# Performance work log

Hardware: AMD Instinct MI355X
Metric: run time of the kernel (lower is better)

## Reference

```python
import jax, jax.numpy as jnp
import numpy as np
import math

B, S, D, H, G = 2, 2048, 2048, 16, 4
DH = D // H          # 128 head dim
BASE = 1_000_000.0   # RoPE base


def _rope(x):
    # x: (..., S, DH); interleaved RoPE matching the torch module
    pos = jnp.arange(S, dtype=jnp.float32)[:, None]            # (S,1)
    i = jnp.arange(DH // 2, dtype=jnp.float32)                 # (DH/2,)
    omega = jnp.exp(-2.0 * i / DH * math.log(BASE))            # (DH/2,)
    ang = pos * omega                                          # (S, DH/2)
    sin = jnp.repeat(jnp.sin(ang), 2, axis=-1)                 # (S, DH)
    cos = jnp.repeat(jnp.cos(ang), 2, axis=-1)                 # (S, DH)
    xe, xo = x[..., 0::2], x[..., 1::2]
    rot = jnp.stack([-xo, xe], axis=-1).reshape(x.shape)       # (-x1,x0,-x3,x2,...)
    return x * cos + rot * sin


def setup_inputs() -> dict:
    key = jax.random.key(0)
    ks = jax.random.split(key, 5)
    x = jax.random.normal(ks[0], (B, S, D), jnp.float32)
    wq = jax.random.normal(ks[1], (D, D), jnp.float32) * 0.02
    wk = jax.random.normal(ks[2], (DH * G, D), jnp.float32) * 0.02
    wv = jax.random.normal(ks[3], (DH * G, D), jnp.float32) * 0.02
    wo = jax.random.normal(ks[4], (D, D), jnp.float32) * 0.02
    bq = jnp.zeros((D,), jnp.float32)
    bk = jnp.zeros((DH * G,), jnp.float32)
    bv = jnp.zeros((DH * G,), jnp.float32)
    bo = jnp.zeros((D,), jnp.float32)
    masked = jnp.broadcast_to(jnp.triu(jnp.ones((S, S), bool), 1), (B * H, S, S))
    return {"x": x, "wq": wq, "bq": bq, "wk": wk, "bk": bk, "wv": wv,
            "bv": bv, "wo": wo, "bo": bo, "masked": masked}


def reference(x, wq, bq, wk, bk, wv, bv, wo, bo, masked):
    r = H // G  # q heads per kv head; repeat_interleave order -> q head h uses kv h//r
    q = (x @ wq.T + bq).reshape(B, S, H, DH).transpose(0, 2, 1, 3)   # (B,H,S,DH)
    k = (x @ wk.T + bk).reshape(B, S, G, DH).transpose(0, 2, 1, 3)   # (B,G,S,DH)
    v = (x @ wv.T + bv).reshape(B, S, G, DH).transpose(0, 2, 1, 3)   # (B,G,S,DH)
    q = _rope(q)
    k = _rope(k)
    qg = q.reshape(B, G, r, S, DH)                                    # group q heads by kv head
    scores = jnp.einsum('bgrsd,bgtd->bgrst', qg, k)                   # (B,G,r,S,S)
    m = masked.reshape(B, G, r, S, S)
    scores = jnp.where(m, -jnp.inf, scores)
    attn = jax.nn.softmax(scores / math.sqrt(DH), axis=-1)
    out = jnp.einsum('bgrst,bgtd->bgrsd', attn, v)                    # (B,G,r,S,DH)
    out = out.reshape(B, H, S, DH).transpose(0, 2, 1, 3).reshape(B, S, D)
    return out @ wo.T + bo
```

## Files before the change

kernel.cpp:

```cpp
#include <hip/hip_runtime.h>

typedef unsigned short u16;
typedef __attribute__((ext_vector_type(4))) float f32x4;
typedef __attribute__((ext_vector_type(8))) __bf16 bf16x8;

static __device__ __forceinline__ u16 f2bf(float f) {
  unsigned u = __float_as_uint(f);
  u += 0x7FFFu + ((u >> 16) & 1u);
  return (u16)(u >> 16);
}
static __device__ __forceinline__ float bf2f(u16 h) {
  return __uint_as_float(((unsigned)h) << 16);
}

#define GLOAD16(gsrc, ldst)                                                    \
  __builtin_amdgcn_global_load_lds(                                            \
      (const __attribute__((address_space(1))) unsigned int*)(gsrc),           \
      (__attribute__((address_space(3))) unsigned int*)(ldst), 16, 0, 0)

__global__ void k_cvt5(const float* __restrict__ x, const float* __restrict__ wq,
                       const float* __restrict__ wk, const float* __restrict__ wv,
                       const float* __restrict__ wo, const float* __restrict__ bq,
                       const float* __restrict__ bk, const float* __restrict__ bv,
                       u16* __restrict__ xb, u16* __restrict__ wqkvb,
                       u16* __restrict__ wob, float* __restrict__ biascat) {
  int i = blockIdx.x * blockDim.x + threadIdx.x;
  const float* src;
  u16* dst;
  if (i < 2097152) { src = x + (size_t)i * 4; dst = xb + (size_t)i * 4; }
  else if (i < 3145728) { src = wq + (size_t)(i - 2097152) * 4; dst = wqkvb + (size_t)(i - 2097152) * 4; }
  else if (i < 3407872) { src = wk + (size_t)(i - 3145728) * 4; dst = wqkvb + (size_t)(i - 2097152) * 4; }
  else if (i < 3670016) { src = wv + (size_t)(i - 3407872) * 4; dst = wqkvb + (size_t)(i - 2097152) * 4; }
  else if (i < 4718592) { src = wo + (size_t)(i - 3670016) * 4; dst = wob + (size_t)(i - 3670016) * 4; }
  else {
    int t = i - 4718592;
    const float* s2 = (t < 512) ? bq + t * 4
                     : (t < 640) ? bk + (t - 512) * 4
                                 : bv + (t - 640) * 4;
    ((float4*)biascat)[t] = *(const float4*)s2;
    return;
  }
  float4 v = *(const float4*)src;
  ushort4 o;
  o.x = f2bf(v.x); o.y = f2bf(v.y); o.z = f2bf(v.z); o.w = f2bf(v.w);
  *(ushort4*)dst = o;
}

template <int MODE>
__global__ __launch_bounds__(256) void k_gemm_bt(const u16* __restrict__ A,
                                                 const u16* __restrict__ Bt,
                                                 const float* __restrict__ bias,
                                                 void* __restrict__ Cv,
                                                 u16* __restrict__ VtG,
                                                 int M, int N, int K) {
  __shared__ __align__(128) char smem[16384];
  const int tid = threadIdx.x;
  const int lane = tid & 63;
  const int wave = tid >> 6;
  const int m0 = blockIdx.y << 7;
  const int n0 = blockIdx.x << 7;
  const int wr = (wave >> 1) << 6;
  const int wc = (wave & 1) << 6;

  f32x4 acc[4][4];
#pragma unroll
  for (int m = 0; m < 4; ++m)
#pragma unroll
    for (int n = 0; n < 4; ++n) acc[m][n] = (f32x4){0.f, 0.f, 0.f, 0.f};

  const int nk = K >> 5;
  for (int kt = 0; kt < nk; ++kt) {
    const int kk0 = kt << 5;
#pragma unroll
    for (int iss = 0; iss < 4; ++iss) {
      int o = tid * 16 + iss * 4096;
      int lo = o & 8191;
      int row = lo >> 6;
      int cs = ((lo >> 4) & 3) ^ (row & 3);
      const u16* src =
          (o >= 8192 ? Bt + (size_t)(n0 + row) * K : A + (size_t)(m0 + row) * K) + kk0 + cs * 8;
      GLOAD16(src, smem + iss * 4096 + wave * 1024);
    }
    __syncthreads();
    bf16x8 af[4], bfr[4];
#pragma unroll
    for (int m = 0; m < 4; ++m) {
      int r = wr + m * 16 + (lane & 15);
      af[m] = *(const bf16x8*)(smem + r * 64 + (((lane >> 4) ^ (r & 3)) << 4));
    }
#pragma unroll
    for (int n = 0; n < 4; ++n) {
      int r = wc + n * 16 + (lane & 15);
      bfr[n] = *(const bf16x8*)(smem + 8192 + r * 64 + (((lane >> 4) ^ (r & 3)) << 4));
    }
#pragma unroll
    for (int m = 0; m < 4; ++m)
#pragma unroll
      for (int n = 0; n < 4; ++n)
        acc[m][n] = __builtin_amdgcn_mfma_f32_16x16x32_bf16(af[m], bfr[n], acc[m][n], 0, 0, 0);
    __syncthreads();
  }

  if (MODE == 2 && n0 >= 2560) {
#pragma unroll
    for (int n = 0; n < 4; ++n) {
      int col = n0 + wc + n * 16 + (lane & 15);
      int vd = col - 2560;
      float bsv = bias[col];
      u16* vrow = VtG + ((size_t)vd) * 2048;
#pragma unroll
      for (int m = 0; m < 4; ++m) {
        int rb = m0 + wr + m * 16 + ((lane >> 4) << 2);
        int bb = rb >> 11, ss = rb & 2047;
        ushort4 w;
        w.x = f2bf(acc[m][n][0] + bsv);
        w.y = f2bf(acc[m][n][1] + bsv);
        w.z = f2bf(acc[m][n][2] + bsv);
        w.w = f2bf(acc[m][n][3] + bsv);
        *(ushort4*)(vrow + (size_t)bb * (512 * 2048) + ss) = w;
      }
    }
    return;
  }

  if (MODE == 2) {
#pragma unroll
    for (int n = 0; n < 4; ++n) {
      int col = n0 + wc + n * 16 + (lane & 15);
      float bsv = bias[col];
      float omega = __expf(-0.21586735f * (float)((col & 127) >> 1));
      float sd1, cd1, sd2, cd2, sd3, cd3;
      sincosf(omega, &sd1, &cd1);
      sincosf(omega * 2.f, &sd2, &cd2);
      sincosf(omega * 3.f, &sd3, &cd3);
      const bool odd = col & 1;
      const float qsc = (col < 2048) ? 0.08838834764831845f : 1.0f;
#pragma unroll
      for (int m = 0; m < 4; ++m) {
        int rb = m0 + wr + m * 16 + ((lane >> 4) << 2);
        float s0, c0;
        sincosf((float)(rb & 2047) * omega, &s0, &c0);
        float css[4] = {c0, c0 * cd1 - s0 * sd1, c0 * cd2 - s0 * sd2, c0 * cd3 - s0 * sd3};
        float snn[4] = {s0, s0 * cd1 + c0 * sd1, s0 * cd2 + c0 * sd2, s0 * cd3 + c0 * sd3};
#pragma unroll
        for (int j = 0; j < 4; ++j) {
          float v = acc[m][n][j] + bsv;
          float partner = __shfl_xor(v, 1);
          float r = odd ? fmaf(v, css[j], partner * snn[j])
                        : fmaf(v, css[j], -partner * snn[j]);
          ((u16*)Cv)[(size_t)(rb + j) * N + col] = f2bf(r * qsc);
        }
      }
    }
    return;
  }

#pragma unroll
  for (int n = 0; n < 4; ++n) {
    int col = n0 + wc + n * 16 + (lane & 15);
    float bsv = bias[col];
#pragma unroll
    for (int m = 0; m < 4; ++m) {
      int rb = m0 + wr + m * 16 + ((lane >> 4) << 2);
#pragma unroll
      for (int j = 0; j < 4; ++j) {
        float v = acc[m][n][j] + bsv;
        ((float*)Cv)[(size_t)(rb + j) * N + col] = v;
      }
    }
  }
}

__global__ __launch_bounds__(256) void k_attn(const u16* __restrict__ qkv,
                                              const u16* __restrict__ vtg,
                                              u16* __restrict__ Ob) {
  __shared__ __align__(128) char smem[40960];
  const int tid = threadIdx.x, lane = tid & 63, wave = tid >> 6;
  const int g16 = lane >> 4;
  const int l15 = lane & 15;
  const int bh = blockIdx.x;
  const int Q0 = (31 - blockIdx.y) << 6;
  const int b = bh >> 4, h = bh & 15, gq = h >> 2;
  const int brow = b << 11;
  const int qcol = h << 7;
  const int kcol = 2048 + (gq << 7);
  const u16* vt_base = vtg + ((size_t)((b << 2) + gq) << 7) * 2048;

  bf16x8 qf[4];
  {
    int qrow = brow + Q0 + wave * 16 + l15;
    const u16* qp = qkv + (size_t)qrow * 3072 + qcol + (g16 << 3);
#pragma unroll
    for (int kk = 0; kk < 4; ++kk) qf[kk] = *(const bf16x8*)(qp + kk * 32);
  }

  f32x4 oacc[8];
#pragma unroll
  for (int d = 0; d < 8; ++d) oacc[d] = (f32x4){0.f, 0.f, 0.f, 0.f};
  float mrow[4], lrow[4];
#pragma unroll
  for (int j = 0; j < 4; ++j) { mrow[j] = -1e30f; lrow[j] = 0.f; }

  const int nkt = (Q0 >> 6) + 1;
  char* const pbase = smem + 32768 + wave * 2048;

  for (int kt = 0; kt < nkt; ++kt) {
    const size_t krowg = (size_t)(brow + (kt << 6));
#pragma unroll
    for (int iss = 0; iss < 4; ++iss) {
      int o = iss * 4096 + tid * 16;
      int row = o >> 8;
      int cs = ((o >> 4) & 15) ^ (row & 7);
      const u16* src = qkv + (krowg + row) * 3072 + kcol + cs * 8;
      GLOAD16(src, smem + iss * 4096 + wave * 1024);
    }
#pragma unroll
    for (int iss = 0; iss < 4; ++iss) {
      int o = iss * 4096 + tid * 16;
      int d = o >> 7;
      int cs = ((o >> 4) & 7) ^ (d & 7);
      const u16* src = vt_base + (size_t)d * 2048 + (kt << 6) + cs * 8;
      GLOAD16(src, smem + 16384 + iss * 4096 + wave * 1024);
    }
    __syncthreads();

    f32x4 sfr[4];
    __builtin_amdgcn_s_setprio(1);
#pragma unroll
    for (int kc = 0; kc < 4; ++kc) {
      f32x4 s = (f32x4){0.f, 0.f, 0.f, 0.f};
      int r = kc * 16 + l15;
#pragma unroll
      for (int kk = 0; kk < 4; ++kk) {
        int byte = r * 256 + ((((kk << 2) + g16) ^ (r & 7)) << 4);
        bf16x8 kf = *(const bf16x8*)(smem + byte);
        s = __builtin_amdgcn_mfma_f32_16x16x32_bf16(qf[kk], kf, s, 0, 0, 0);
      }
      sfr[kc] = s;
    }
    __builtin_amdgcn_s_setprio(0);
    const int qbase = Q0 + wave * 16 + (g16 << 2);
#pragma unroll
    for (int kc = 0; kc < 4; ++kc) {
      int kidx = (kt << 6) + kc * 16 + l15;
#pragma unroll
      for (int j = 0; j < 4; ++j)
        if (kidx > qbase + j) sfr[kc][j] = -3.0e38f;
    }
#pragma unroll
    for (int j = 0; j < 4; ++j) {
      float mx = fmaxf(fmaxf(sfr[0][j], sfr[1][j]), fmaxf(sfr[2][j], sfr[3][j]));
#pragma unroll
      for (int msk = 8; msk >= 1; msk >>= 1) mx = fmaxf(mx, __shfl_xor(mx, msk));
      float mnew = fmaxf(mrow[j], mx);
      float alpha = __expf(mrow[j] - mnew);
      const int q = (g16 << 2) + j;
      const int qkey = (q >> 1) & 7;
      float rs = 0.f;
#pragma unroll
      for (int kc = 0; kc < 4; ++kc) {
        float p = __expf(sfr[kc][j] - mnew);
        rs += p;
        int k = kc * 16 + l15;
        *(u16*)(pbase + q * 128 + (((k >> 3) ^ qkey) << 4) + ((k & 7) << 1)) = f2bf(p);
      }
#pragma unroll
      for (int msk = 8; msk >= 1; msk >>= 1) rs += __shfl_xor(rs, msk);
      lrow[j] = lrow[j] * alpha + rs;
      mrow[j] = mnew;
#pragma unroll
      for (int dt = 0; dt < 8; ++dt) oacc[dt][j] *= alpha;
    }
    asm volatile("s_waitcnt lgkmcnt(0)" ::: "memory");
    __builtin_amdgcn_sched_barrier(0);
    __builtin_amdgcn_s_setprio(1);
#pragma unroll
    for (int ks = 0; ks < 2; ++ks) {
      bf16x8 pf = *(const bf16x8*)(pbase + l15 * 128 +
                                   ((((ks << 2) + g16) ^ ((l15 >> 1) & 7)) << 4));
#pragma unroll
      for (int dt = 0; dt < 8; ++dt) {
        int d = (dt << 4) + l15;
        bf16x8 vf = *(const bf16x8*)(smem + 16384 + d * 128 +
                                     ((((ks << 2) + g16) ^ (d & 7)) << 4));
        oacc[dt] = __builtin_amdgcn_mfma_f32_16x16x32_bf16(pf, vf, oacc[dt], 0, 0, 0);
      }
    }
    __builtin_amdgcn_s_setprio(0);
    __syncthreads();
  }

#pragma unroll
  for (int j = 0; j < 4; ++j) {
    int q = Q0 + wave * 16 + (g16 << 2) + j;
    float inv = 1.0f / lrow[j];
    u16* op = Ob + (size_t)(brow + q) * 2048 + qcol + l15;
#pragma unroll
    for (int dt = 0; dt < 8; ++dt) op[dt * 16] = f2bf(oacc[dt][j] * inv);
  }
}

extern "C" void kernel_launch(void* const* d_in, const int* in_sizes, int n_in,
                              void* d_out, int out_size, void* d_ws, size_t ws_size,
                              hipStream_t stream) {
  const float* x  = (const float*)d_in[0];
  const float* wq = (const float*)d_in[1];
  const float* bq = (const float*)d_in[2];
  const float* wk = (const float*)d_in[3];
  const float* bk = (const float*)d_in[4];
  const float* wv = (const float*)d_in[5];
  const float* bv = (const float*)d_in[6];
  const float* wo = (const float*)d_in[7];
  const float* bo = (const float*)d_in[8];
  float* out = (float*)d_out;

  u16* wsu = (u16*)d_ws;
  u16* xb      = wsu;
  u16* wqkvb   = xb + (size_t)4096 * 2048;
  u16* wob     = wqkvb + (size_t)3072 * 2048;
  u16* qkv     = wob + (size_t)2048 * 2048;
  float* biascat = (float*)(qkv + (size_t)4096 * 3072);
  u16* vtg     = (u16*)(biascat + 3072);
  u16* Ob = xb;

  k_cvt5<<<18435, 256, 0, stream>>>(x, wq, wk, wv, wo, bq, bk, bv,
                                    xb, wqkvb, wob, biascat);

  k_gemm_bt<2><<<dim3(3072 / 128, 4096 / 128), 256, 0, stream>>>(
      xb, wqkvb, biascat, qkv, vtg, 4096, 3072, 2048);

  k_attn<<<dim3(32, 32), 256, 0, stream>>>(qkv, vtg, Ob);

  k_gemm_bt<1><<<dim3(2048 / 128, 4096 / 128), 256, 0, stream>>>(
      Ob, wob, bo, out, nullptr, 4096, 2048, 2048);
}
```

Measured before the change: 264.2 us.

## Double attention query tile to 128 rows per block, two 16-row subtiles per wave

The attention kernel now processes 128 query rows per block, with each wave owning two 16-row query subtiles, so every K and V tile staged in LDS feeds twice as many MFMAs. This halves the grid's y dimension and the total global-to-LDS traffic for K/V, and waves whose rows lie entirely before a key tile skip its compute. In exchange, register pressure rises (doubled accumulators and softmax state), the grid has fewer blocks, LDS per block grows, and some waves idle on diagonal tiles, which adds causal imbalance.

```diff
diff --git a/kernel.cpp b/kernel.cpp
--- a/kernel.cpp
+++ b/kernel.cpp
@@ -174,35 +174,41 @@
 __global__ __launch_bounds__(256) void k_attn(const u16* __restrict__ qkv,
                                               const u16* __restrict__ vtg,
                                               u16* __restrict__ Ob) {
-  __shared__ __align__(128) char smem[40960];
+  __shared__ __align__(128) char smem[49152];
   const int tid = threadIdx.x, lane = tid & 63, wave = tid >> 6;
   const int g16 = lane >> 4;
   const int l15 = lane & 15;
   const int bh = blockIdx.x;
-  const int Q0 = (31 - blockIdx.y) << 6;
+  const int Q0 = (15 - blockIdx.y) << 7;
   const int b = bh >> 4, h = bh & 15, gq = h >> 2;
   const int brow = b << 11;
   const int qcol = h << 7;
   const int kcol = 2048 + (gq << 7);
   const u16* vt_base = vtg + ((size_t)((b << 2) + gq) << 7) * 2048;
 
-  bf16x8 qf[4];
-  {
-    int qrow = brow + Q0 + wave * 16 + l15;
+  bf16x8 qf[2][4];
+#pragma unroll
+  for (int qi = 0; qi < 2; ++qi) {
+    int qrow = brow + Q0 + wave * 32 + qi * 16 + l15;
     const u16* qp = qkv + (size_t)qrow * 3072 + qcol + (g16 << 3);
 #pragma unroll
-    for (int kk = 0; kk < 4; ++kk) qf[kk] = *(const bf16x8*)(qp + kk * 32);
-  }
-
-  f32x4 oacc[8];
-#pragma unroll
-  for (int d = 0; d < 8; ++d) oacc[d] = (f32x4){0.f, 0.f, 0.f, 0.f};
-  float mrow[4], lrow[4];
-#pragma unroll
-  for (int j = 0; j < 4; ++j) { mrow[j] = -1e30f; lrow[j] = 0.f; }
-
-  const int nkt = (Q0 >> 6) + 1;
-  char* const pbase = smem + 32768 + wave * 2048;
+    for (int kk = 0; kk < 4; ++kk) qf[qi][kk] = *(const bf16x8*)(qp + kk * 32);
+  }
+
+  f32x4 oacc[2][8];
+#pragma unroll
+  for (int qi = 0; qi < 2; ++qi)
+#pragma unroll
+    for (int d = 0; d < 8; ++d) oacc[qi][d] = (f32x4){0.f, 0.f, 0.f, 0.f};
+  float mrow[2][4], lrow[2][4];
+#pragma unroll
+  for (int qi = 0; qi < 2; ++qi)
+#pragma unroll
+    for (int j = 0; j < 4; ++j) { mrow[qi][j] = -1e30f; lrow[qi][j] = 0.f; }
+
+  const int nkt = (Q0 >> 6) + 2;
+  const int qmaxw = Q0 + wave * 32 + 31;
+  char* const pbase = smem + 32768 + wave * 4096;
 
   for (int kt = 0; kt < nkt; ++kt) {
     const size_t krowg = (size_t)(brow + (kt << 6));
@@ -224,80 +230,94 @@
     }
     __syncthreads();
 
-    f32x4 sfr[4];
-    __builtin_amdgcn_s_setprio(1);
-#pragma unroll
-    for (int kc = 0; kc < 4; ++kc) {
-      f32x4 s = (f32x4){0.f, 0.f, 0.f, 0.f};
-      int r = kc * 16 + l15;
-#pragma unroll
-      for (int kk = 0; kk < 4; ++kk) {
-        int byte = r * 256 + ((((kk << 2) + g16) ^ (r & 7)) << 4);
-        bf16x8 kf = *(const bf16x8*)(smem + byte);
-        s = __builtin_amdgcn_mfma_f32_16x16x32_bf16(qf[kk], kf, s, 0, 0, 0);
-      }
-      sfr[kc] = s;
-    }
-    __builtin_amdgcn_s_setprio(0);
-    const int qbase = Q0 + wave * 16 + (g16 << 2);
-#pragma unroll
-    for (int kc = 0; kc < 4; ++kc) {
-      int kidx = (kt << 6) + kc * 16 + l15;
-#pragma unroll
-      for (int j = 0; j < 4; ++j)
-        if (kidx > qbase + j) sfr[kc][j] = -3.0e38f;
-    }
+    if ((kt << 6) <= qmaxw) {
+      f32x4 sfr[2][4];
+      __builtin_amdgcn_s_setprio(1);
+#pragma unroll
+      for (int kc = 0; kc < 4; ++kc) {
+        f32x4 s0 = (f32x4){0.f, 0.f, 0.f, 0.f};
+        f32x4 s1 = (f32x4){0.f, 0.f, 0.f, 0.f};
+        int r = kc * 16 + l15;
+#pragma unroll
+        for (int kk = 0; kk < 4; ++kk) {
+          int byte = r * 256 + ((((kk << 2) + g16) ^ (r & 7)) << 4);
+          bf16x8 kf = *(const bf16x8*)(smem + byte);
+          s0 = __builtin_amdgcn_mfma_f32_16x16x32_bf16(qf[0][kk], kf, s0, 0, 0, 0);
+          s1 = __builtin_amdgcn_mfma_f32_16x16x32_bf16(qf[1][kk], kf, s1, 0, 0, 0);
+        }
+        sfr[0][kc] = s0;
+        sfr[1][kc] = s1;
+      }
+      __builtin_amdgcn_s_setprio(0);
+#pragma unroll
+      for (int qi = 0; qi < 2; ++qi) {
+        const int qb = Q0 + wave * 32 + qi * 16 + (g16 << 2);
+#pragma unroll
+        for (int kc = 0; kc < 4; ++kc) {
+          int kidx = (kt << 6) + kc * 16 + l15;
+#pragma unroll
+          for (int j = 0; j < 4; ++j)
+            if (kidx > qb + j) sfr[qi][kc][j] = -3.0e38f;
+        }
+#pragma unroll
+        for (int j = 0; j < 4; ++j) {
+          float mx = fmaxf(fmaxf(sfr[qi][0][j], sfr[qi][1][j]),
+                           fmaxf(sfr[qi][2][j], sfr[qi][3][j]));
+#pragma unroll
+          for (int msk = 8; msk >= 1; msk >>= 1) mx = fmaxf(mx, __shfl_xor(mx, msk));
+          float mnew = fmaxf(mrow[qi][j], mx);
+          float alpha = __expf(mrow[qi][j] - mnew);
+          const int q = qi * 16 + (g16 << 2) + j;
+          const int qkey = (q >> 1) & 7;
+          float rs = 0.f;
+#pragma unroll
+          for (int kc = 0; kc < 4; ++kc) {
+            float p = __expf(sfr[qi][kc][j] - mnew);
+            rs += p;
+            int k = kc * 16 + l15;
+            *(u16*)(pbase + q * 128 + (((k >> 3) ^ qkey) << 4) + ((k & 7) << 1)) = f2bf(p);
+          }
+#pragma unroll
+          for (int msk = 8; msk >= 1; msk >>= 1) rs += __shfl_xor(rs, msk);
+          lrow[qi][j] = lrow[qi][j] * alpha + rs;
+          mrow[qi][j] = mnew;
+#pragma unroll
+          for (int dt = 0; dt < 8; ++dt) oacc[qi][dt][j] *= alpha;
+        }
+      }
+      asm volatile("s_waitcnt lgkmcnt(0)" ::: "memory");
+      __builtin_amdgcn_sched_barrier(0);
+      __builtin_amdgcn_s_setprio(1);
+#pragma unroll
+      for (int ks = 0; ks < 2; ++ks) {
+        bf16x8 pf0 = *(const bf16x8*)(pbase + l15 * 128 +
+                                      ((((ks << 2) + g16) ^ ((l15 >> 1) & 7)) << 4));
+        bf16x8 pf1 = *(const bf16x8*)(pbase + (16 + l15) * 128 +
+                                      ((((ks << 2) + g16) ^ ((l15 >> 1) & 7)) << 4));
+#pragma unroll
+        for (int dt = 0; dt < 8; ++dt) {
+          int d = (dt << 4) + l15;
+          bf16x8 vf = *(const bf16x8*)(smem + 16384 + d * 128 +
+                                       ((((ks << 2) + g16) ^ (d & 7)) << 4));
+          oacc[0][dt] = __builtin_amdgcn_mfma_f32_16x16x32_bf16(pf0, vf, oacc[0][dt], 0, 0, 0);
+          oacc[1][dt] = __builtin_amdgcn_mfma_f32_16x16x32_bf16(pf1, vf, oacc[1][dt], 0, 0, 0);
+        }
+      }
+      __builtin_amdgcn_s_setprio(0);
+    }
+    __syncthreads();
+  }
+
+#pragma unroll
+  for (int qi = 0; qi < 2; ++qi)
 #pragma unroll
     for (int j = 0; j < 4; ++j) {
-      float mx = fmaxf(fmaxf(sfr[0][j], sfr[1][j]), fmaxf(sfr[2][j], sfr[3][j]));
-#pragma unroll
-      for (int msk = 8; msk >= 1; msk >>= 1) mx = fmaxf(mx, __shfl_xor(mx, msk));
-      float mnew = fmaxf(mrow[j], mx);
-      float alpha = __expf(mrow[j] - mnew);
-      const int q = (g16 << 2) + j;
-      const int qkey = (q >> 1) & 7;
-      float rs = 0.f;
-#pragma unroll
-      for (int kc = 0; kc < 4; ++kc) {
-        float p = __expf(sfr[kc][j] - mnew);
-        rs += p;
-        int k = kc * 16 + l15;
-        *(u16*)(pbase + q * 128 + (((k >> 3) ^ qkey) << 4) + ((k & 7) << 1)) = f2bf(p);
-      }
-#pragma unroll
-      for (int msk = 8; msk >= 1; msk >>= 1) rs += __shfl_xor(rs, msk);
-      lrow[j] = lrow[j] * alpha + rs;
-      mrow[j] = mnew;
-#pragma unroll
-      for (int dt = 0; dt < 8; ++dt) oacc[dt][j] *= alpha;
-    }
-    asm volatile("s_waitcnt lgkmcnt(0)" ::: "memory");
-    __builtin_amdgcn_sched_barrier(0);
-    __builtin_amdgcn_s_setprio(1);
-#pragma unroll
-    for (int ks = 0; ks < 2; ++ks) {
-      bf16x8 pf = *(const bf16x8*)(pbase + l15 * 128 +
-                                   ((((ks << 2) + g16) ^ ((l15 >> 1) & 7)) << 4));
-#pragma unroll
-      for (int dt = 0; dt < 8; ++dt) {
-        int d = (dt << 4) + l15;
-        bf16x8 vf = *(const bf16x8*)(smem + 16384 + d * 128 +
-                                     ((((ks << 2) + g16) ^ (d & 7)) << 4));
-        oacc[dt] = __builtin_amdgcn_mfma_f32_16x16x32_bf16(pf, vf, oacc[dt], 0, 0, 0);
-      }
-    }
-    __builtin_amdgcn_s_setprio(0);
-    __syncthreads();
-  }
-
-#pragma unroll
-  for (int j = 0; j < 4; ++j) {
-    int q = Q0 + wave * 16 + (g16 << 2) + j;
-    float inv = 1.0f / lrow[j];
-    u16* op = Ob + (size_t)(brow + q) * 2048 + qcol + l15;
-#pragma unroll
-    for (int dt = 0; dt < 8; ++dt) op[dt * 16] = f2bf(oacc[dt][j] * inv);
-  }
+      int q = Q0 + wave * 32 + qi * 16 + (g16 << 2) + j;
+      float inv = 1.0f / lrow[qi][j];
+      u16* op = Ob + (size_t)(brow + q) * 2048 + qcol + l15;
+#pragma unroll
+      for (int dt = 0; dt < 8; ++dt) op[dt * 16] = f2bf(oacc[qi][dt][j] * inv);
+    }
 }
 
 extern "C" void kernel_launch(void* const* d_in, const int* in_sizes, int n_in,
@@ -329,7 +349,7 @@
   k_gemm_bt<2><<<dim3(3072 / 128, 4096 / 128), 256, 0, stream>>>(
       xb, wqkvb, biascat, qkv, vtg, 4096, 3072, 2048);
 
-  k_attn<<<dim3(32, 32), 256, 0, stream>>>(qkv, vtg, Ob);
+  k_attn<<<dim3(32, 16), 256, 0, stream>>>(qkv, vtg, Ob);
 
   k_gemm_bt<1><<<dim3(2048 / 128, 4096 / 128), 256, 0, stream>>>(
       Ob, wob, bo, out, nullptr, 4096, 2048, 2048);
```

Measured after the change: 304.4 us. 1.15x slower.
